# Performance work log

Measured on AMD Instinct MI355X. Metric: run time of the kernel, lower is better.

## Reference

```python
import jax, jax.numpy as jnp
import numpy as np

VOCAB = 32000
EMB = 512
HID = 1024
OUT = 2

def setup_inputs() -> dict:
    key = jax.random.key(0)
    ks = jax.random.split(key, 8)
    stdv = 1.0 / np.sqrt(HID)
    x = jax.random.randint(ks[0], (512, 128), 0, VOCAB)
    emb = jax.random.normal(ks[1], (VOCAB, EMB), dtype=jnp.float32)
    w_ih = jax.random.uniform(ks[2], (4 * HID, EMB), minval=-stdv, maxval=stdv, dtype=jnp.float32)
    w_hh = jax.random.uniform(ks[3], (4 * HID, HID), minval=-stdv, maxval=stdv, dtype=jnp.float32)
    b_ih = jax.random.uniform(ks[4], (4 * HID,), minval=-stdv, maxval=stdv, dtype=jnp.float32)
    b_hh = jax.random.uniform(ks[5], (4 * HID,), minval=-stdv, maxval=stdv, dtype=jnp.float32)
    fc_w = jax.random.normal(ks[6], (OUT, HID), dtype=jnp.float32) * 0.02
    fc_b = jnp.zeros((OUT,), dtype=jnp.float32)
    return {"x": x, "emb": emb, "w_ih": w_ih, "w_hh": w_hh,
            "b_ih": b_ih, "b_hh": b_hh, "fc_w": fc_w, "fc_b": fc_b}

def reference(x, emb, w_ih, w_hh, b_ih, b_hh, fc_w, fc_b):
    T, B = x.shape
    embedded = emb[x]  # [T, B, EMB]
    # precompute input projections for all steps: [T, B, 4H]
    x_gates = jnp.einsum('tbe,ge->tbg', embedded, w_ih) + b_ih + b_hh
    h0 = jnp.zeros((B, HID), dtype=embedded.dtype)
    c0 = jnp.zeros((B, HID), dtype=embedded.dtype)

    def step(carry, xg):
        hx, cx = carry
        gates = xg + hx @ w_hh.T  # [B, 4H]
        i, f, g, o = jnp.split(gates, 4, axis=1)
        i = jax.nn.sigmoid(i)
        f = jax.nn.sigmoid(f)
        g = jnp.tanh(g)
        o = jax.nn.sigmoid(o)
        cy = f * cx + i * g
        hy = o * jnp.tanh(cy)
        return (hy, cy), hy

    (hT, cT), all_h = jax.lax.scan(step, (h0, c0), x_gates)
    out = hT @ fc_w.T + fc_b  # [B, OUT]
    return out
```

## Files before the change

### kernel.cpp

```cpp
#include <hip/hip_runtime.h>

typedef short short8 __attribute__((ext_vector_type(8)));
typedef float f32x4 __attribute__((ext_vector_type(4)));
typedef unsigned long long u64;

#define T_STEPS 512
#define BATCH   128
#define EMBD    512
#define HID     1024
#define NWG     256
#define NTHR    1024
#define NGROUP  8
#define WPG     32

#define SLOT_STRIDE 16
#define SLOT_BYTES  (NWG * SLOT_STRIDE * 4)
#define H_OFF     SLOT_BYTES
#define H_BYTES   (NGROUP * 2 * 16384 * 2)
#define WH_OFF    (H_OFF + H_BYTES)
#define WH_BYTES  (32u*32u*8u*64u*8u*2u)
#define WI_OFF    (WH_OFF + WH_BYTES)
#define WI_BYTES  (32u*16u*8u*64u*8u*2u)
#define BS_OFF    (WI_OFF + WI_BYTES)
#define BS_BYTES  (4096 * 4)
#define PT_OFF    (BS_OFF + BS_BYTES)
#define PT_BYTES  (BATCH * 32 * 2 * 4)
#define EMB_OFF   (PT_OFF + PT_BYTES)
#define EMB_BYTES ((size_t)T_STEPS*16*8*64*8*2)
#define WS_NEEDED (EMB_OFF + EMB_BYTES)

__device__ __forceinline__ unsigned short f2b(float f) {
    unsigned u = __builtin_bit_cast(unsigned, f);
    u += 0x7FFFu + ((u >> 16) & 1u);
    return (unsigned short)(u >> 16);
}

__device__ __forceinline__ uint4 pack8(float4 a, float4 b) {
    uint4 r;
    r.x = (unsigned)f2b(a.x) | ((unsigned)f2b(a.y) << 16);
    r.y = (unsigned)f2b(a.z) | ((unsigned)f2b(a.w) << 16);
    r.z = (unsigned)f2b(b.x) | ((unsigned)f2b(b.y) << 16);
    r.w = (unsigned)f2b(b.z) | ((unsigned)f2b(b.w) << 16);
    return r;
}

__device__ __forceinline__ float fsig(float x) {
    float e = __expf(-fabsf(x));
    float r = 1.f / (1.f + e);
    return x >= 0.f ? r : 1.f - r;
}
__device__ __forceinline__ float ftanh_(float x) {
    float e = __expf(-2.f * fabsf(x));
    float r = (1.f - e) / (1.f + e);
    return x >= 0.f ? r : -r;
}

__global__ void prep_wh(const float* __restrict__ w_hh, unsigned short* __restrict__ wh_arr) {
    int gid = blockIdx.x * blockDim.x + threadIdx.x;
    int l  = gid & 63;
    int nq = (gid >> 6) & 7;
    int ks = (gid >> 9) & 31;
    int w  = gid >> 14;
    int lr = nq * 16 + (l & 15);
    int grow = (lr >> 5) * HID + w * 32 + (lr & 31);
    int k = ks * 32 + (l >> 4) * 8;
    const float4* src = reinterpret_cast<const float4*>(w_hh + (size_t)grow * HID + k);
    *reinterpret_cast<uint4*>(wh_arr + (size_t)gid * 8) = pack8(src[0], src[1]);
}

__global__ void prep_wi(const float* __restrict__ w_ih, unsigned short* __restrict__ wi_arr) {
    int gid = blockIdx.x * blockDim.x + threadIdx.x;
    int l  = gid & 63;
    int nq = (gid >> 6) & 7;
    int eks = (gid >> 9) & 15;
    int w  = gid >> 13;
    int lr = nq * 16 + (l & 15);
    int grow = (lr >> 5) * HID + w * 32 + (lr & 31);
    int k = eks * 32 + (l >> 4) * 8;
    const float4* src = reinterpret_cast<const float4*>(w_ih + (size_t)grow * EMBD + k);
    *reinterpret_cast<uint4*>(wi_arr + (size_t)gid * 8) = pack8(src[0], src[1]);
}

__global__ void prep_bsum(const float* __restrict__ b_ih, const float* __restrict__ b_hh,
                          float* __restrict__ bs) {
    int gid = blockIdx.x * blockDim.x + threadIdx.x;
    int w = gid >> 7, lr = gid & 127;
    int grow = (lr >> 5) * HID + w * 32 + (lr & 31);
    bs[gid] = b_ih[grow] + b_hh[grow];
}

__global__ void prep_emb(const int* __restrict__ x, const float* __restrict__ emb,
                         unsigned short* __restrict__ emb_arr) {
    int gid = blockIdx.x * blockDim.x + threadIdx.x;
    int l  = gid & 63;
    int mt = (gid >> 6) & 7;
    int ks = (gid >> 9) & 15;
    int t  = gid >> 13;
    int b  = mt * 16 + (l & 15);
    int k  = ks * 32 + (l >> 4) * 8;
    int tok = x[t * BATCH + b];
    const float4* src = reinterpret_cast<const float4*>(emb + (size_t)tok * EMBD + k);
    *reinterpret_cast<uint4*>(emb_arr + (size_t)gid * 8) = pack8(src[0], src[1]);
}

__global__ __launch_bounds__(NTHR) void lstm_main(
    const unsigned short* __restrict__ wh_arr,
    const unsigned short* __restrict__ wi_arr,
    const float* __restrict__ bs_arr,
    const unsigned short* __restrict__ emb_arr,
    unsigned short* __restrict__ h_arr,
    const float* __restrict__ fc_w,
    float* __restrict__ partials,
    unsigned* __restrict__ slots)
{
    __shared__ __align__(16) unsigned short wis[16 * 8 * 64 * 8];
    __shared__ __align__(16) char ovl[32768];
    float*  gbuf   = reinterpret_cast<float*>(ovl);
    unsigned short* stage = reinterpret_cast<unsigned short*>(ovl);
    u64*    stage64 = reinterpret_cast<u64*>(ovl);

    const int tid  = threadIdx.x;
    const int wgid = blockIdx.x;
    const int g = wgid >> 5;
    const int w = wgid & 31;

    {
        const uint4* s2 = reinterpret_cast<const uint4*>(wi_arr + (size_t)w * 65536);
        uint4* d2 = reinterpret_cast<uint4*>(wis);
        for (int i = tid; i < 8192; i += NTHR) d2[i] = s2[i];
    }

    const int lane = tid & 63;
    const int wave = tid >> 6;
    const int nq   = wave >> 1;
    const int kq   = wave & 1;

    short8 bh[16];
    #pragma unroll
    for (int s = 0; s < 16; ++s) {
        int ks = kq * 16 + s;
        bh[s] = *reinterpret_cast<const short8*>(wh_arr + (size_t)(((w * 32 + ks) * 8 + nq) * 64 + lane) * 8);
    }

    const int pb = tid >> 4;
    const int cp = tid & 15;
    const int c0 = cp * 2, c1 = cp * 2 + 1;
    float bi0[4], bi1[4];
    if (tid < 256) {
        #pragma unroll
        for (int gm = 0; gm < 4; ++gm) {
            bi0[gm] = bs_arr[w * 128 + gm * 32 + c0];
            bi1[gm] = bs_arr[w * 128 + gm * 32 + c1];
        }
    }
    __syncthreads();

    const int lrD   = nq * 16 + (lane & 15);
    const int rbase = (lane >> 4) * 4;
    const int lane2 = ((cp >> 2) << 4) | pb;
    const int hidx32 = (w * 64 + lane2) * 4 + (cp & 3);

    float c0s = 0.f, c1s = 0.f, h0r = 0.f, h1r = 0.f;

    for (int t = 0; t < T_STEPS; ++t) {
        f32x4 acc = {0.f, 0.f, 0.f, 0.f};

        const unsigned short* ebuf = emb_arr + (size_t)t * 65536;
        #pragma unroll
        for (int s = 0; s < 8; ++s) {
            int eks = kq * 8 + s;
            short8 a  = *reinterpret_cast<const short8*>(ebuf + ((eks * 8 + g) * 64 + lane) * 8);
            short8 bw = *reinterpret_cast<const short8*>(wis + ((eks * 8 + nq) * 64 + lane) * 8);
            acc = __builtin_amdgcn_mfma_f32_16x16x32_bf16(a, bw, acc, 0, 0, 0);
        }

        if (t > 0) {
            if (tid < WPG) {
                while (__hip_atomic_load(&slots[(g * WPG + tid) * SLOT_STRIDE],
                                         __ATOMIC_RELAXED, __HIP_MEMORY_SCOPE_AGENT) < (unsigned)t) {}
            }
            __syncthreads();
            asm volatile("" ::: "memory");
            const u64* hs = reinterpret_cast<const u64*>(h_arr + (size_t)(g * 2 + (t & 1)) * 16384);
            #pragma unroll
            for (int q = 0; q < 4; ++q) {
                u64 v = __hip_atomic_load(hs + q * 1024 + tid, __ATOMIC_RELAXED, __HIP_MEMORY_SCOPE_AGENT);
                stage64[q * 1024 + tid] = v;
            }
            __syncthreads();
            #pragma unroll
            for (int s = 0; s < 16; ++s) {
                int ks = kq * 16 + s;
                short8 a = *reinterpret_cast<const short8*>(stage + (ks * 64 + lane) * 8);
                acc = __builtin_amdgcn_mfma_f32_16x16x32_bf16(a, bh[s], acc, 0, 0, 0);
            }
        }
        __syncthreads();

        #pragma unroll
        for (int jj = 0; jj < 4; ++jj)
            gbuf[kq * 2112 + (rbase + jj) * 132 + lrD] = acc[jj];
        __syncthreads();

        if (tid < 256) {
            const float* g0 = gbuf + pb * 132;
            const float* g1 = gbuf + 2112 + pb * 132;
            float xi0 = g0[c0]      + g1[c0]      + bi0[0];
            float xf0 = g0[32 + c0] + g1[32 + c0] + bi0[1];
            float xg0 = g0[64 + c0] + g1[64 + c0] + bi0[2];
            float xo0 = g0[96 + c0] + g1[96 + c0] + bi0[3];
            float xi1 = g0[c1]      + g1[c1]      + bi1[0];
            float xf1 = g0[32 + c1] + g1[32 + c1] + bi1[1];
            float xg1 = g0[64 + c1] + g1[64 + c1] + bi1[2];
            float xo1 = g0[96 + c1] + g1[96 + c1] + bi1[3];
            float i0 = fsig(xi0), f0 = fsig(xf0), gg0 = ftanh_(xg0), o0 = fsig(xo0);
            float i1 = fsig(xi1), f1 = fsig(xf1), gg1 = ftanh_(xg1), o1 = fsig(xo1);
            c0s = f0 * c0s + i0 * gg0;
            c1s = f1 * c1s + i1 * gg1;
            h0r = o0 * ftanh_(c0s);
            h1r = o1 * ftanh_(c1s);
            unsigned pk = (unsigned)f2b(h0r) | ((unsigned)f2b(h1r) << 16);
            unsigned* hd = reinterpret_cast<unsigned*>(h_arr + (size_t)(g * 2 + ((t + 1) & 1)) * 16384);
            __hip_atomic_store(hd + hidx32, pk, __ATOMIC_RELAXED, __HIP_MEMORY_SCOPE_AGENT);
        }
        __syncthreads();
        if (tid == 0) {
            __hip_atomic_store(&slots[(g * WPG + w) * SLOT_STRIDE], (unsigned)(t + 1),
                               __ATOMIC_RELEASE, __HIP_MEMORY_SCOPE_AGENT);
        }
    }

    if (tid < 256) {
        int col0 = w * 32 + c0, col1 = w * 32 + c1;
        float v0 = h0r * fc_w[col0] + h1r * fc_w[col1];
        float v1 = h0r * fc_w[HID + col0] + h1r * fc_w[HID + col1];
        #pragma unroll
        for (int m = 1; m < 16; m <<= 1) {
            v0 += __shfl_xor(v0, m);
            v1 += __shfl_xor(v1, m);
        }
        if (cp == 0) {
            partials[((g * 16 + pb) * 32 + w) * 2 + 0] = v0;
            partials[((g * 16 + pb) * 32 + w) * 2 + 1] = v1;
        }
    }
}

__global__ void finalize(const float* __restrict__ partials, const float* __restrict__ fc_b,
                         float* __restrict__ out) {
    int tid = threadIdx.x;
    int b = tid >> 1, o = tid & 1;
    float s = fc_b[o];
    for (int w = 0; w < 32; ++w) s += partials[(b * 32 + w) * 2 + o];
    out[b * 2 + o] = s;
}

extern "C" void kernel_launch(void* const* d_in, const int* in_sizes, int n_in,
                              void* d_out, int out_size, void* d_ws, size_t ws_size,
                              hipStream_t stream) {
    const int*   x    = (const int*)d_in[0];
    const float* emb  = (const float*)d_in[1];
    const float* w_ih = (const float*)d_in[2];
    const float* w_hh = (const float*)d_in[3];
    const float* b_ih = (const float*)d_in[4];
    const float* b_hh = (const float*)d_in[5];
    const float* fc_w = (const float*)d_in[6];
    const float* fc_b = (const float*)d_in[7];
    float* out = (float*)d_out;
    char* ws = (char*)d_ws;

    if (ws_size < WS_NEEDED) {
        (void)hipMemsetAsync(d_out, 0xFF, (size_t)out_size * sizeof(float), stream);
        return;
    }

    unsigned*       slots   = (unsigned*)(ws);
    unsigned short* h_arr   = (unsigned short*)(ws + H_OFF);
    unsigned short* wh_arr  = (unsigned short*)(ws + WH_OFF);
    unsigned short* wi_arr  = (unsigned short*)(ws + WI_OFF);
    float*          bs_arr  = (float*)(ws + BS_OFF);
    float*          pt_arr  = (float*)(ws + PT_OFF);
    unsigned short* emb_arr = (unsigned short*)(ws + EMB_OFF);

    (void)hipMemsetAsync(ws, 0, SLOT_BYTES, stream);

    prep_wh  <<<2048, 256, 0, stream>>>(w_hh, wh_arr);
    prep_wi  <<<1024, 256, 0, stream>>>(w_ih, wi_arr);
    prep_bsum<<<16,   256, 0, stream>>>(b_ih, b_hh, bs_arr);
    prep_emb <<<16384,256, 0, stream>>>(x, emb, emb_arr);
    lstm_main<<<NWG, NTHR, 0, stream>>>(wh_arr, wi_arr, bs_arr, emb_arr, h_arr,
                                        fc_w, pt_arr, slots);
    finalize <<<1, 256, 0, stream>>>(pt_arr, fc_b, out);
}
```

Before: 3.667 ms.

## Use hierarchical group barrier and LLC-bypass loads/stores for recurrent hidden state exchange

Only workgroup 0 of each group polls all 32 peer slots, then publishes a single group-ready flag that the other workgroups spin on. Hidden-state loads and stores now use sc0 sc1 global instructions with explicit vmcnt waits, and the release store on the slot becomes relaxed. The bias is folded into the accumulator init, and the gate epilogue uses 128 threads with float4 reads. This is meant to cut polling traffic and per-step latency on the serial critical path, but it adds an extra hop through the leader and relies on the cache-bypass flags for memory ordering.

Measured after the change: 3.858 ms. 5.2% more time.

```diff
diff --git a/kernel.cpp b/kernel.cpp
--- a/kernel.cpp
+++ b/kernel.cpp
@@ -2,7 +2,8 @@
 
 typedef short short8 __attribute__((ext_vector_type(8)));
 typedef float f32x4 __attribute__((ext_vector_type(4)));
-typedef unsigned long long u64;
+typedef unsigned int u32x4 __attribute__((ext_vector_type(4)));
+typedef unsigned int u32x2 __attribute__((ext_vector_type(2)));
 
 #define T_STEPS 512
 #define BATCH   128
@@ -15,8 +16,10 @@
 
 #define SLOT_STRIDE 16
 #define SLOT_BYTES  (NWG * SLOT_STRIDE * 4)
-#define H_OFF     SLOT_BYTES
-#define H_BYTES   (NGROUP * 2 * 16384 * 2)
+#define GR_OFF    SLOT_BYTES
+#define GR_BYTES  1024
+#define H_OFF     (SLOT_BYTES + GR_BYTES)
+#define H_BYTES   (NGROUP * 2 * 32768)
 #define WH_OFF    (H_OFF + H_BYTES)
 #define WH_BYTES  (32u*32u*8u*64u*8u*2u)
 #define WI_OFF    (WH_OFF + WH_BYTES)
@@ -53,6 +56,16 @@
     float e = __expf(-2.f * fabsf(x));
     float r = (1.f - e) / (1.f + e);
     return x >= 0.f ? r : -r;
+}
+
+__device__ __forceinline__ void llc_load16(const void* p, u32x4& v) {
+    asm volatile("global_load_dwordx4 %0, %1, off sc0 sc1" : "=v"(v) : "v"(p));
+}
+__device__ __forceinline__ void llc_store8(void* p, u32x2 v) {
+    asm volatile("global_store_dwordx2 %0, %1, off sc0 sc1" :: "v"(p), "v"(v) : "memory");
+}
+__device__ __forceinline__ void waitvm0() {
+    asm volatile("s_waitcnt vmcnt(0)" ::: "memory");
 }
 
 __global__ void prep_wh(const float* __restrict__ w_hh, unsigned short* __restrict__ wh_arr) {
@@ -115,9 +128,11 @@
 {
     __shared__ __align__(16) unsigned short wis[16 * 8 * 64 * 8];
     __shared__ __align__(16) char ovl[32768];
-    float*  gbuf   = reinterpret_cast<float*>(ovl);
+    float* gbf    = reinterpret_cast<float*>(ovl);
+    u32x4* stage4 = reinterpret_cast<u32x4*>(ovl);
     unsigned short* stage = reinterpret_cast<unsigned short*>(ovl);
-    u64*    stage64 = reinterpret_cast<u64*>(ovl);
+
+    unsigned* gr = slots + (GR_OFF >> 2);
 
     const int tid  = threadIdx.x;
     const int wgid = blockIdx.x;
@@ -142,28 +157,19 @@
         bh[s] = *reinterpret_cast<const short8*>(wh_arr + (size_t)(((w * 32 + ks) * 8 + nq) * 64 + lane) * 8);
     }
 
-    const int pb = tid >> 4;
-    const int cp = tid & 15;
-    const int c0 = cp * 2, c1 = cp * 2 + 1;
-    float bi0[4], bi1[4];
-    if (tid < 256) {
-        #pragma unroll
-        for (int gm = 0; gm < 4; ++gm) {
-            bi0[gm] = bs_arr[w * 128 + gm * 32 + c0];
-            bi1[gm] = bs_arr[w * 128 + gm * 32 + c1];
-        }
-    }
-    __syncthreads();
-
     const int lrD   = nq * 16 + (lane & 15);
     const int rbase = (lane >> 4) * 4;
-    const int lane2 = ((cp >> 2) << 4) | pb;
-    const int hidx32 = (w * 64 + lane2) * 4 + (cp & 3);
-
-    float c0s = 0.f, c1s = 0.f, h0r = 0.f, h1r = 0.f;
+    const float bini = (kq == 0) ? bs_arr[w * 128 + lrD] : 0.f;
+
+    const int pb = tid & 15;
+    const int qd = tid >> 4;
+    float cs[4] = {0.f, 0.f, 0.f, 0.f};
+    float hr[4] = {0.f, 0.f, 0.f, 0.f};
+
+    __syncthreads();
 
     for (int t = 0; t < T_STEPS; ++t) {
-        f32x4 acc = {0.f, 0.f, 0.f, 0.f};
+        f32x4 acc = {bini, bini, bini, bini};
 
         const unsigned short* ebuf = emb_arr + (size_t)t * 65536;
         #pragma unroll
@@ -175,19 +181,33 @@
         }
 
         if (t > 0) {
-            if (tid < WPG) {
-                while (__hip_atomic_load(&slots[(g * WPG + tid) * SLOT_STRIDE],
-                                         __ATOMIC_RELAXED, __HIP_MEMORY_SCOPE_AGENT) < (unsigned)t) {}
+            if (w == 0) {
+                if (tid < WPG) {
+                    while (__hip_atomic_load(&slots[(g * WPG + tid) * SLOT_STRIDE],
+                                             __ATOMIC_RELAXED, __HIP_MEMORY_SCOPE_AGENT) < (unsigned)t) {}
+                }
+                asm volatile("" ::: "memory");
+                if (tid == 0)
+                    __hip_atomic_store(&gr[g * 32], (unsigned)t,
+                                       __ATOMIC_RELAXED, __HIP_MEMORY_SCOPE_AGENT);
+            } else {
+                if (tid == 0) {
+                    while (__hip_atomic_load(&gr[g * 32],
+                                             __ATOMIC_RELAXED, __HIP_MEMORY_SCOPE_AGENT) < (unsigned)t) {}
+                }
             }
             __syncthreads();
-            asm volatile("" ::: "memory");
-            const u64* hs = reinterpret_cast<const u64*>(h_arr + (size_t)(g * 2 + (t & 1)) * 16384);
-            #pragma unroll
-            for (int q = 0; q < 4; ++q) {
-                u64 v = __hip_atomic_load(hs + q * 1024 + tid, __ATOMIC_RELAXED, __HIP_MEMORY_SCOPE_AGENT);
-                stage64[q * 1024 + tid] = v;
-            }
+
+            const char* hb = reinterpret_cast<const char*>(h_arr) + (size_t)(g * 2 + (t & 1)) * 32768;
+            u32x4 v0, v1;
+            llc_load16(hb + tid * 16, v0);
+            llc_load16(hb + (tid + 1024) * 16, v1);
+            waitvm0();
+            __builtin_amdgcn_sched_barrier(0);
+            stage4[tid] = v0;
+            stage4[tid + 1024] = v1;
             __syncthreads();
+
             #pragma unroll
             for (int s = 0; s < 16; ++s) {
                 int ks = kq * 16 + s;
@@ -199,50 +219,64 @@
 
         #pragma unroll
         for (int jj = 0; jj < 4; ++jj)
-            gbuf[kq * 2112 + (rbase + jj) * 132 + lrD] = acc[jj];
+            gbf[kq * 2112 + (rbase + jj) * 132 + lrD] = acc[jj];
         __syncthreads();
 
-        if (tid < 256) {
-            const float* g0 = gbuf + pb * 132;
-            const float* g1 = gbuf + 2112 + pb * 132;
-            float xi0 = g0[c0]      + g1[c0]      + bi0[0];
-            float xf0 = g0[32 + c0] + g1[32 + c0] + bi0[1];
-            float xg0 = g0[64 + c0] + g1[64 + c0] + bi0[2];
-            float xo0 = g0[96 + c0] + g1[96 + c0] + bi0[3];
-            float xi1 = g0[c1]      + g1[c1]      + bi1[0];
-            float xf1 = g0[32 + c1] + g1[32 + c1] + bi1[1];
-            float xg1 = g0[64 + c1] + g1[64 + c1] + bi1[2];
-            float xo1 = g0[96 + c1] + g1[96 + c1] + bi1[3];
-            float i0 = fsig(xi0), f0 = fsig(xf0), gg0 = ftanh_(xg0), o0 = fsig(xo0);
-            float i1 = fsig(xi1), f1 = fsig(xf1), gg1 = ftanh_(xg1), o1 = fsig(xo1);
-            c0s = f0 * c0s + i0 * gg0;
-            c1s = f1 * c1s + i1 * gg1;
-            h0r = o0 * ftanh_(c0s);
-            h1r = o1 * ftanh_(c1s);
-            unsigned pk = (unsigned)f2b(h0r) | ((unsigned)f2b(h1r) << 16);
-            unsigned* hd = reinterpret_cast<unsigned*>(h_arr + (size_t)(g * 2 + ((t + 1) & 1)) * 16384);
-            __hip_atomic_store(hd + hidx32, pk, __ATOMIC_RELAXED, __HIP_MEMORY_SCOPE_AGENT);
+        if (tid < 128) {
+            const float* g0 = gbf + pb * 132;
+            const float* g1 = gbf + 2112 + pb * 132;
+            const int cb = qd * 4;
+            float4 xi = *reinterpret_cast<const float4*>(g0 + cb);
+            float4 xf = *reinterpret_cast<const float4*>(g0 + 32 + cb);
+            float4 xg = *reinterpret_cast<const float4*>(g0 + 64 + cb);
+            float4 xo = *reinterpret_cast<const float4*>(g0 + 96 + cb);
+            float4 yi = *reinterpret_cast<const float4*>(g1 + cb);
+            float4 yf = *reinterpret_cast<const float4*>(g1 + 32 + cb);
+            float4 yg = *reinterpret_cast<const float4*>(g1 + 64 + cb);
+            float4 yo = *reinterpret_cast<const float4*>(g1 + 96 + cb);
+            float ti[4] = {xi.x + yi.x, xi.y + yi.y, xi.z + yi.z, xi.w + yi.w};
+            float tf[4] = {xf.x + yf.x, xf.y + yf.y, xf.z + yf.z, xf.w + yf.w};
+            float tg[4] = {xg.x + yg.x, xg.y + yg.y, xg.z + yg.z, xg.w + yg.w};
+            float to[4] = {xo.x + yo.x, xo.y + yo.y, xo.z + yo.z, xo.w + yo.w};
+            #pragma unroll
+            for (int e = 0; e < 4; ++e) {
+                float ig = fsig(ti[e]), fg = fsig(tf[e]), gg = ftanh_(tg[e]), og = fsig(to[e]);
+                cs[e] = fg * cs[e] + ig * gg;
+                hr[e] = og * ftanh_(cs[e]);
+            }
+            u32x2 pk;
+            pk.x = (unsigned)f2b(hr[0]) | ((unsigned)f2b(hr[1]) << 16);
+            pk.y = (unsigned)f2b(hr[2]) | ((unsigned)f2b(hr[3]) << 16);
+            char* hd = reinterpret_cast<char*>(h_arr) + (size_t)(g * 2 + ((t + 1) & 1)) * 32768;
+            llc_store8(hd + (w * 64 + (qd >> 1) * 16 + pb) * 16 + (qd & 1) * 8, pk);
+            waitvm0();
         }
         __syncthreads();
         if (tid == 0) {
             __hip_atomic_store(&slots[(g * WPG + w) * SLOT_STRIDE], (unsigned)(t + 1),
-                               __ATOMIC_RELEASE, __HIP_MEMORY_SCOPE_AGENT);
-        }
-    }
-
-    if (tid < 256) {
-        int col0 = w * 32 + c0, col1 = w * 32 + c1;
-        float v0 = h0r * fc_w[col0] + h1r * fc_w[col1];
-        float v1 = h0r * fc_w[HID + col0] + h1r * fc_w[HID + col1];
+                               __ATOMIC_RELAXED, __HIP_MEMORY_SCOPE_AGENT);
+        }
+    }
+
+    __syncthreads();
+    float* red = reinterpret_cast<float*>(ovl);
+    if (tid < 128) {
+        float v0 = 0.f, v1 = 0.f;
         #pragma unroll
-        for (int m = 1; m < 16; m <<= 1) {
-            v0 += __shfl_xor(v0, m);
-            v1 += __shfl_xor(v1, m);
-        }
-        if (cp == 0) {
-            partials[((g * 16 + pb) * 32 + w) * 2 + 0] = v0;
-            partials[((g * 16 + pb) * 32 + w) * 2 + 1] = v1;
-        }
+        for (int e = 0; e < 4; ++e) {
+            int col = w * 32 + qd * 4 + e;
+            v0 += hr[e] * fc_w[col];
+            v1 += hr[e] * fc_w[HID + col];
+        }
+        red[tid * 2]     = v0;
+        red[tid * 2 + 1] = v1;
+    }
+    __syncthreads();
+    if (tid < 32) {
+        int b = tid >> 1, o = tid & 1;
+        float s = 0.f;
+        for (int q = 0; q < 8; ++q) s += red[((q << 4) | b) * 2 + o];
+        partials[((g * 16 + b) * 32 + w) * 2 + o] = s;
     }
 }
 
@@ -282,7 +316,7 @@
     float*          pt_arr  = (float*)(ws + PT_OFF);
     unsigned short* emb_arr = (unsigned short*)(ws + EMB_OFF);
 
-    (void)hipMemsetAsync(ws, 0, SLOT_BYTES, stream);
+    (void)hipMemsetAsync(ws, 0, SLOT_BYTES + GR_BYTES, stream);
 
     prep_wh  <<<2048, 256, 0, stream>>>(w_hh, wh_arr);
     prep_wi  <<<1024, 256, 0, stream>>>(w_ih, wi_arr);
```
